# Performance work log

Measured on AMD Instinct MI355X. Metric: run time of the kernel, lower is better.

## Reference

```python
import jax, jax.numpy as jnp
import numpy as np

N_TOKENS = 2048
HIDDEN = 1024
INTER = 2816
N_EXPERTS = 8
N_ADAPTERS = 2
MAX_RANK = 16
TOP_K = 2
N_SEQS = 8


def setup_inputs() -> dict:
    key = jax.random.key(0)
    ks = jax.random.split(key, 12)
    f32 = jnp.float32
    std = 0.02
    hidden_states = jax.random.normal(ks[0], (N_TOKENS, HIDDEN), f32)
    topk_ids = jax.random.randint(ks[1], (N_TOKENS, TOP_K), 0, N_EXPERTS)
    tw = jax.random.uniform(ks[2], (N_TOKENS, TOP_K), dtype=f32)
    topk_weights = tw / tw.sum(axis=-1, keepdims=True)
    gate_a = jax.random.normal(ks[3], (N_ADAPTERS, N_EXPERTS, MAX_RANK, HIDDEN), f32) * std
    gate_b = jax.random.normal(ks[4], (N_ADAPTERS, N_EXPERTS, INTER, MAX_RANK), f32) * std
    up_a = jax.random.normal(ks[5], (N_ADAPTERS, N_EXPERTS, MAX_RANK, HIDDEN), f32) * std
    up_b = jax.random.normal(ks[6], (N_ADAPTERS, N_EXPERTS, INTER, MAX_RANK), f32) * std
    down_a = jax.random.normal(ks[7], (N_ADAPTERS, N_EXPERTS, MAX_RANK, INTER), f32) * std
    down_b = jax.random.normal(ks[8], (N_ADAPTERS, N_EXPERTS, HIDDEN, MAX_RANK), f32) * std
    weight_indices = jax.random.randint(ks[9], (N_SEQS,), 0, N_ADAPTERS)
    seq_lens = jnp.full((N_SEQS,), N_TOKENS // N_SEQS, dtype=jnp.int32)
    lora_ranks = jnp.array([16, 8], dtype=jnp.int32)
    scalings = jnp.array([2.0, 1.0], dtype=f32)
    base_gate_up_weight = jax.random.normal(ks[10], (N_EXPERTS, 2 * INTER, HIDDEN), f32) * std
    base_down_weight = jax.random.normal(ks[11], (N_EXPERTS, HIDDEN, INTER), f32) * std
    return {
        'hidden_states': hidden_states, 'topk_ids': topk_ids, 'topk_weights': topk_weights,
        'gate_a': gate_a, 'gate_b': gate_b, 'up_a': up_a, 'up_b': up_b,
        'down_a': down_a, 'down_b': down_b, 'weight_indices': weight_indices,
        'seq_lens': seq_lens, 'lora_ranks': lora_ranks, 'scalings': scalings,
        'base_gate_up_weight': base_gate_up_weight, 'base_down_weight': base_down_weight,
    }


def _forward(hidden_states, topk_ids, topk_weights, gate_a, gate_b, up_a, up_b,
             down_a, down_b, weight_indices, seq_lens, lora_ranks, scalings,
             base_gate_up_weight, base_down_weight):
    N, H = hidden_states.shape
    A, E, R, _ = gate_a.shape
    I = gate_b.shape[2]
    x = hidden_states.astype(jnp.float32)
    # token -> sequence -> adapter (replaces the per-token python loop)
    token_to_seq = jnp.searchsorted(jnp.cumsum(seq_lens), jnp.arange(N), side='right')
    adapter = weight_indices[token_to_seq]                               # [N]
    scale_t = scalings[adapter].astype(jnp.float32)[:, None]             # [N,1]
    # per-adapter rank truncation A[:rank] == zeroing rows r >= rank of LoRA-A
    rmask = (jnp.arange(R)[None, :] < lora_ranks[:, None]).astype(jnp.float32)  # [A,R]
    ga = gate_a.astype(jnp.float32) * rmask[:, None, :, None]
    ua = up_a.astype(jnp.float32) * rmask[:, None, :, None]
    da = down_a.astype(jnp.float32) * rmask[:, None, :, None]
    gb = gate_b.astype(jnp.float32)
    ub = up_b.astype(jnp.float32)
    db = down_b.astype(jnp.float32)
    # low-rank input projections for all adapters & experts (tiny: N*A*E*R)
    z_gate = jnp.einsum('nh,aerh->naer', x, ga)
    z_up = jnp.einsum('nh,aerh->naer', x, ua)
    sel = adapter[:, None, None]
    Wgu = base_gate_up_weight.astype(jnp.float32)   # [E, 2I, H]
    Wd = base_down_weight.astype(jnp.float32)       # [E, H, I]
    out = jnp.zeros((N, H), jnp.float32)
    for e in range(E):
        # summed routing weight for this expert per token (0 => no contribution)
        w_e = jnp.where(topk_ids == e, topk_weights, 0.0).sum(axis=1).astype(jnp.float32)  # [N]
        base_gate = x @ Wgu[e, :I].T                 # [N,I]
        base_up = x @ Wgu[e, I:].T                   # [N,I]
        lg = jnp.take_along_axis(jnp.einsum('nar,air->nai', z_gate[:, :, e], gb[:, e]), sel, axis=1)[:, 0]
        lu = jnp.take_along_axis(jnp.einsum('nar,air->nai', z_up[:, :, e], ub[:, e]), sel, axis=1)[:, 0]
        gate_out = base_gate + scale_t * lg
        up_out = base_up + scale_t * lu
        act = jax.nn.silu(gate_out) * up_out         # [N,I]
        zd = jnp.einsum('ni,ari->nar', act, da[:, e])
        ld = jnp.take_along_axis(jnp.einsum('nar,ahr->nah', zd, db[:, e]), sel, axis=1)[:, 0]
        base_down = act @ Wd[e].T                    # [N,H]
        out = out + w_e[:, None] * (base_down + scale_t * ld)
    return out.astype(hidden_states.dtype)


def reference(hidden_states, topk_ids, topk_weights, gate_a, gate_b, up_a, up_b,
              down_a, down_b, weight_indices, seq_lens, lora_ranks, scalings,
              base_gate_up_weight, base_down_weight):
    return _forward(hidden_states, topk_ids, topk_weights, gate_a, gate_b, up_a, up_b,
                    down_a, down_b, weight_indices, seq_lens, lora_ranks, scalings,
                    base_gate_up_weight, base_down_weight)
```

## Files before the change

kernel.cpp:

```cpp
#include <hip/hip_runtime.h>
#include <hip/hip_bf16.h>
#include <math.h>

#define N_TOK   2048
#define HIDDEN  1024
#define INTER   2816
#define NEXP    8
#define NADAPT  2
#define MAXRANK 16
#define TOPK    2
#define NSEQ    8
#define NPAIRS  (N_TOK*TOPK)
#define NGU     (2*INTER)

typedef unsigned short u16;
typedef __attribute__((ext_vector_type(8))) short bf16x8;
typedef __attribute__((ext_vector_type(4))) float f32x4;

#define F_CNT   0u
#define F_PERM  4096u
#define F_ZG    139264u
#define F_ZU    401408u
#define F_ZD    663552u
#define F_XBF   1048576u
#define F_ACT   5242880u
#define F_GB    28311552u
#define F_UB    29753344u
#define F_DB    31195136u
#define F_GA_BF 31719424u
#define F_UA_BF 32243712u
#define F_ZDF   32768000u
#define F_DA_BF 33554432u
#define FAST_NEED 171966464u

#define B_CNT   0u
#define B_PERM  4096u
#define B_ZG    262144u
#define B_ZU    524288u
#define B_ZD    786432u
#define B_ACT   1048576u

__device__ __forceinline__ float bf2f(u16 u){
  union { unsigned int i; float f; } v; v.i = ((unsigned int)u)<<16; return v.f;
}
__device__ __forceinline__ u16 f2bf(float f){
  union { float f; unsigned int i; } v; v.f = f;
  unsigned int i = v.i;
  return (u16)((i + 0x7fffu + ((i>>16)&1u)) >> 16);
}
__device__ __forceinline__ uint4 cvt8(const float* src){
  float4 lo = *(const float4*)src;
  float4 hi = *(const float4*)(src+4);
  uint4 r;
  r.x = (unsigned)f2bf(lo.x) | ((unsigned)f2bf(lo.y)<<16);
  r.y = (unsigned)f2bf(lo.z) | ((unsigned)f2bf(lo.w)<<16);
  r.z = (unsigned)f2bf(hi.x) | ((unsigned)f2bf(hi.y)<<16);
  r.w = (unsigned)f2bf(hi.z) | ((unsigned)f2bf(hi.w)<<16);
  return r;
}
__device__ __forceinline__ uint2 cvt4(float4 v){
  uint2 r;
  r.x = (unsigned)f2bf(v.x) | ((unsigned)f2bf(v.y)<<16);
  r.y = (unsigned)f2bf(v.z) | ((unsigned)f2bf(v.w)<<16);
  return r;
}

__device__ __forceinline__ unsigned cvtpk(float a, float b){
  unsigned r;
  asm("v_cvt_pk_bf16_f32 %0, %1, %2" : "=v"(r) : "v"(a), "v"(b));
  return r;
}
__device__ __forceinline__ uint4 pack8(float4 lo, float4 hi){
  uint4 r;
  r.x = cvtpk(lo.x, lo.y);
  r.y = cvtpk(lo.z, lo.w);
  r.z = cvtpk(hi.x, hi.y);
  r.w = cvtpk(hi.z, hi.w);
  return r;
}

__device__ __forceinline__ void cvt_chunk8k(const float* __restrict__ src, u16* __restrict__ dst, int c, int t){
  size_t b4 = (size_t)c*2048 + t;
  float4 v0 = ((const float4*)src)[b4];
  float4 v1 = ((const float4*)src)[b4 + 256];
  float4 v2 = ((const float4*)src)[b4 + 512];
  float4 v3 = ((const float4*)src)[b4 + 768];
  float4 v4 = ((const float4*)src)[b4 + 1024];
  float4 v5 = ((const float4*)src)[b4 + 1280];
  float4 v6 = ((const float4*)src)[b4 + 1536];
  float4 v7 = ((const float4*)src)[b4 + 1792];
  ((uint2*)dst)[b4]        = cvt4(v0);
  ((uint2*)dst)[b4 + 256]  = cvt4(v1);
  ((uint2*)dst)[b4 + 512]  = cvt4(v2);
  ((uint2*)dst)[b4 + 768]  = cvt4(v3);
  ((uint2*)dst)[b4 + 1024] = cvt4(v4);
  ((uint2*)dst)[b4 + 1280] = cvt4(v5);
  ((uint2*)dst)[b4 + 1536] = cvt4(v6);
  ((uint2*)dst)[b4 + 1792] = cvt4(v7);
}
__device__ __forceinline__ void zero_chunk8k(float* dst, int c, int t){
  size_t b4 = (size_t)c*2048 + t;
  #pragma unroll
  for (int i = 0; i < 8; ++i)
    ((float4*)dst)[b4 + i*256] = make_float4(0.f,0.f,0.f,0.f);
}

__device__ __forceinline__ void gl16(const void* g, void* l){
  __builtin_amdgcn_global_load_lds(
      (const __attribute__((address_space(1))) unsigned int*)g,
      (__attribute__((address_space(3))) unsigned int*)l, 16, 0, 0);
}

__device__ __forceinline__ int token_adapter(int n, const int* seq_lens, const int* widx){
  int cum = 0;
  #pragma unroll
  for (int s = 0; s < NSEQ; ++s){ cum += seq_lens[s]; if (n < cum) return widx[s]; }
  return widx[NSEQ-1];
}

__global__ void k_zero(float* outf, int* cnt, float* zdf){
  int t = threadIdx.x;
  if (blockIdx.x < 2048){
    int id = blockIdx.x*256 + t;
    *(float4*)&outf[(size_t)id*4] = make_float4(0.f,0.f,0.f,0.f);
  } else {
    int id = (blockIdx.x - 2048)*256 + t;
    *(float4*)&zdf[(size_t)id*4] = make_float4(0.f,0.f,0.f,0.f);
  }
  if (blockIdx.x == 0 && t < NEXP) cnt[t] = 0;
}

__global__ void k_route(const int* __restrict__ topk_ids, int* cnt, int* perm){
  int p = blockIdx.x*256 + threadIdx.x;
  if (p >= NPAIRS) return;
  int e = topk_ids[p];
  int pos = atomicAdd(&cnt[e], 1);
  perm[e*NPAIRS + pos] = p;
}

__global__ void k_cvt(const float* __restrict__ src, u16* __restrict__ dst, int n4){
  int id = blockIdx.x*256 + threadIdx.x;
  if (id >= n4) return;
  ((uint2*)dst)[id] = cvt4(((const float4*)src)[id]);
}

__global__ void k_prep(
    const float* __restrict__ x,  const float* __restrict__ gb, const float* __restrict__ ub,
    const float* __restrict__ ga, const float* __restrict__ ua, const float* __restrict__ db_,
    const float* __restrict__ da,
    u16* xb, u16* gbb, u16* ubb, u16* gab, u16* uab, u16* dbb, u16* dab,
    float* outf, float* zdf, int* cnt)
{
  int b = blockIdx.x, t = threadIdx.x;
  if (b == 0 && t < NEXP) cnt[t] = 0;
  if      (b < 256) cvt_chunk8k(x,   xb,  b,       t);
  else if (b < 344) cvt_chunk8k(gb,  gbb, b - 256, t);
  else if (b < 432) cvt_chunk8k(ub,  ubb, b - 344, t);
  else if (b < 464) cvt_chunk8k(ga,  gab, b - 432, t);
  else if (b < 496) cvt_chunk8k(ua,  uab, b - 464, t);
  else if (b < 528) cvt_chunk8k(db_, dbb, b - 496, t);
  else if (b < 616) cvt_chunk8k(da,  dab, b - 528, t);
  else if (b < 872) zero_chunk8k(outf, b - 616, t);
  else              zero_chunk8k(zdf,  b - 872, t);
}

__global__ __launch_bounds__(256) void k_zgu_mfma(
    const u16* __restrict__ xb, const u16* __restrict__ gab, const u16* __restrict__ uab,
    const int* __restrict__ cnt, const int* __restrict__ perm,
    const int* __restrict__ widx, const int* __restrict__ seq_lens,
    const int* __restrict__ ranks, const float* __restrict__ scal,
    u16* __restrict__ zg, u16* __restrict__ zu)
{
  int e = blockIdx.y;
  int me = cnt[e];
  int tm = blockIdx.x;
  if (tm*64 >= me) return;
  int t = threadIdx.x;

  __shared__ __align__(16) u16 As[64*32];
  __shared__ __align__(16) u16 Bs[64*32];

  int r0 = t >> 2;
  int kc = ((t&3) - r0) & 3;
  int ko = kc*8;
  int mg = tm*64 + r0;
  int pa = perm[e*NPAIRS + min(mg, me-1)];
  const u16* arow = xb + (size_t)(pa>>1)*HIDDEN + ko;
  int jr = r0 & 31;
  const u16* brow = (r0 < 32 ? gab : uab)
                    + (size_t)(((jr>>4)*NEXP + e)*MAXRANK + (jr&15))*HIDDEN + ko;

  int wv = t>>6, lane = t&63;
  u16* Asw = &As[wv*512];
  u16* Bsw = &Bs[wv*512];
  int wm = wv>>1, wn = wv&1;
  int l15 = lane&15, q = lane>>4;

  f32x4 acc[2][2] = {};
  int aoff[2], boff[2];
  #pragma unroll
  for (int i=0;i<2;++i){ int row = wm*32 + i*16 + l15; aoff[i] = row*32 + ((q+row)&3)*8; }
  #pragma unroll
  for (int j=0;j<2;++j){ int row = wn*32 + j*16 + l15; boff[j] = row*32 + ((q+row)&3)*8; }

  for (int kt = 0; kt < HIDDEN/32; ++kt){
    __syncthreads();
    gl16(arow + kt*32, Asw);
    gl16(brow + kt*32, Bsw);
    __syncthreads();
    bf16x8 af[2], bfr[2];
    #pragma unroll
    for (int i=0;i<2;++i) af[i] = *(const bf16x8*)&As[aoff[i]];
    #pragma unroll
    for (int j=0;j<2;++j) bfr[j] = *(const bf16x8*)&Bs[boff[j]];
    #pragma unroll
    for (int i=0;i<2;++i)
      #pragma unroll
      for (int j=0;j<2;++j)
        acc[i][j] = __builtin_amdgcn_mfma_f32_16x16x32_bf16(af[i], bfr[j], acc[i][j],0,0,0);
  }

  u16* dstz = wn ? zu : zg;
  #pragma unroll
  for (int i=0;i<2;++i){
    #pragma unroll
    for (int r=0;r<4;++r){
      int mgo = tm*64 + wm*32 + i*16 + q*4 + r;
      if (mgo < me){
        int p = perm[e*NPAIRS + mgo];
        int a = token_adapter(p>>1, seq_lens, widx);
        int rank = ranks[a]; float sc = scal[a];
        #pragma unroll
        for (int j=0;j<2;++j){
          int jc = j*16 + l15;
          float v = ((jc>>4)==a && (jc&15)<rank) ? sc*acc[i][j][r] : 0.f;
          dstz[(size_t)p*32 + jc] = f2bf(v);
        }
      }
    }
  }
}

__global__ __launch_bounds__(256) void k_zd_mfma(
    const u16* __restrict__ act, const u16* __restrict__ dab,
    const int* __restrict__ cnt, const int* __restrict__ perm,
    const int* __restrict__ widx, const int* __restrict__ seq_lens,
    const int* __restrict__ ranks, const float* __restrict__ scal,
    float* __restrict__ zdf)
{
  int e = blockIdx.z;
  int me = cnt[e];
  int tm = blockIdx.y;
  if (tm*64 >= me) return;
  int ks = blockIdx.x;
  int t = threadIdx.x;

  __shared__ __align__(16) u16 As[64*32];
  __shared__ __align__(16) u16 Bs[32*32];

  int r0 = t >> 2;
  int kc = ((t&3) - r0) & 3;
  int ko = kc*8;
  int mg = tm*64 + r0;
  int pa = perm[e*NPAIRS + min(mg, me-1)];
  const u16* arow = act + (size_t)pa*INTER + ko;
  int jr = r0 & 31;
  const u16* brow = dab + (size_t)(((jr>>4)*NEXP + e)*MAXRANK + (jr&15))*INTER + ko;

  int wv = t>>6, lane = t&63;
  u16* Asw = &As[wv*512];
  u16* Bsw = &Bs[(wv&1)*512];
  int l15 = lane&15, q = lane>>4;

  f32x4 acc[2] = {};
  int aoff; { int row = wv*16 + l15; aoff = row*32 + ((q+row)&3)*8; }
  int boff[2];
  #pragma unroll
  for (int j=0;j<2;++j){ int row = j*16 + l15; boff[j] = row*32 + ((q+row)&3)*8; }

  int kt0 = ks*22, kt1 = kt0 + 22;
  for (int kt = kt0; kt < kt1; ++kt){
    __syncthreads();
    gl16(arow + kt*32, Asw);
    if (wv < 2) gl16(brow + kt*32, Bsw);
    __syncthreads();
    bf16x8 af = *(const bf16x8*)&As[aoff];
    bf16x8 b0 = *(const bf16x8*)&Bs[boff[0]];
    bf16x8 b1 = *(const bf16x8*)&Bs[boff[1]];
    acc[0] = __builtin_amdgcn_mfma_f32_16x16x32_bf16(af, b0, acc[0],0,0,0);
    acc[1] = __builtin_amdgcn_mfma_f32_16x16x32_bf16(af, b1, acc[1],0,0,0);
  }

  #pragma unroll
  for (int r=0;r<4;++r){
    int mgo = tm*64 + wv*16 + q*4 + r;
    if (mgo < me){
      int p = perm[e*NPAIRS + mgo];
      int a = token_adapter(p>>1, seq_lens, widx);
      int rank = ranks[a]; float sc = scal[a];
      #pragma unroll
      for (int j=0;j<2;++j){
        int jc = j*16 + l15;
        if ((jc>>4)==a && (jc&15)<rank)
          atomicAdd(&zdf[(size_t)p*32 + jc], sc*acc[j][r]);
      }
    }
  }
}

__global__ __launch_bounds__(256) void k_zgu(
    const float* __restrict__ x, const int* __restrict__ topk_ids,
    const float* __restrict__ gate_a, const float* __restrict__ up_a,
    const int* __restrict__ widx, const int* __restrict__ seq_lens,
    const int* __restrict__ ranks, const float* __restrict__ scal,
    u16* __restrict__ zg, u16* __restrict__ zu)
{
  int p = blockIdx.x, n = p >> 1, t = threadIdx.x;
  int e = topk_ids[p];
  __shared__ float xs[HIDDEN];
  for (int i = t; i < HIDDEN; i += 256) xs[i] = x[(size_t)n*HIDDEN + i];
  if (t < 32){ zg[p*32 + t] = 0; zu[p*32 + t] = 0; }
  __syncthreads();
  int a = token_adapter(n, seq_lens, widx);
  int rank = ranks[a];
  float scale = scal[a];
  int wv = t >> 6, lane = t & 63;
  for (int i = 0; i < 8; ++i){
    int o = wv*8 + i;
    int r = o & 15;
    const float* wrow = ((o < 16) ? gate_a : up_a) + (size_t)((a*NEXP + e)*MAXRANK + r)*HIDDEN;
    float s = 0.f;
    for (int h = lane; h < HIDDEN; h += 64) s += xs[h] * wrow[h];
    s += __shfl_down(s,32); s += __shfl_down(s,16); s += __shfl_down(s,8);
    s += __shfl_down(s,4);  s += __shfl_down(s,2);  s += __shfl_down(s,1);
    if (lane == 0 && r < rank)
      (o < 16 ? zg : zu)[p*32 + a*16 + r] = f2bf(scale * s);
  }
}

__global__ __launch_bounds__(256) void k_zd(
    const u16* __restrict__ act, const int* __restrict__ topk_ids,
    const float* __restrict__ down_a,
    const int* __restrict__ widx, const int* __restrict__ seq_lens,
    const int* __restrict__ ranks, const float* __restrict__ scal,
    u16* __restrict__ zd)
{
  int p = blockIdx.x, n = p >> 1, t = threadIdx.x;
  int e = topk_ids[p];
  __shared__ float as_[INTER];
  for (int i = t; i < INTER; i += 256) as_[i] = bf2f(act[(size_t)p*INTER + i]);
  if (t < 32) zd[p*32 + t] = 0;
  __syncthreads();
  int a = token_adapter(n, seq_lens, widx);
  int rank = ranks[a];
  float scale = scal[a];
  int wv = t >> 6, lane = t & 63;
  for (int i = 0; i < 4; ++i){
    int r = wv*4 + i;
    const float* wrow = down_a + (size_t)((a*NEXP + e)*MAXRANK + r)*INTER;
    float s = 0.f;
    for (int h = lane; h < INTER; h += 64) s += as_[h] * wrow[h];
    s += __shfl_down(s,32); s += __shfl_down(s,16); s += __shfl_down(s,8);
    s += __shfl_down(s,4);  s += __shfl_down(s,2);  s += __shfl_down(s,1);
    if (lane == 0 && r < rank) zd[p*32 + a*16 + r] = f2bf(scale * s);
  }
}

__global__ __launch_bounds__(256) void k_gu_f32(
    const u16* __restrict__ xb, const float* __restrict__ wgu_f32,
    const u16* __restrict__ gbb, const u16* __restrict__ ubb,
    const u16* __restrict__ zg, const u16* __restrict__ zu,
    const int* __restrict__ cnt, const int* __restrict__ perm,
    u16* __restrict__ act)
{
  int e = blockIdx.z;
  int me = cnt[e];
  int tm = blockIdx.y;
  if (tm*128 >= me) return;
  int tn = blockIdx.x;
  int t = threadIdx.x;

  __shared__ __align__(16) u16 As[128*32];
  __shared__ __align__(16) u16 Bg[64*32];
  __shared__ __align__(16) u16 Bu[64*32];

  int r0 = t >> 2;
  int kc = ((t&3) - r0) & 3;
  int ko = kc*8;
  int mg0 = tm*128 + r0, mg1 = mg0 + 64;
  int p0 = perm[e*NPAIRS + min(mg0, me-1)];
  int p1 = perm[e*NPAIRS + min(mg1, me-1)];
  const u16* arow0 = xb + (size_t)(p0>>1)*HIDDEN + ko;
  const u16* arow1 = xb + (size_t)(p1>>1)*HIDDEN + ko;
  int jg = tn*64 + r0;
  const float4* pg = (const float4*)(wgu_f32 + ((size_t)e*NGU + jg)*HIDDEN + ko);
  const float4* pu = (const float4*)(wgu_f32 + ((size_t)e*NGU + INTER + jg)*HIDDEN + ko);

  int wvb = (t>>6)*512;
  u16* Asw0 = &As[wvb];
  u16* Asw1 = &As[2048 + wvb];
  u16* Bgw  = &Bg[wvb];

  int wv = t>>6, lane = t&63;
  int wm = wv>>1, wn = wv&1;
  int l15 = lane&15, q = lane>>4;

  f32x4 accg[4][2] = {};
  f32x4 accu[4][2] = {};
  int aoff[4], boff[2];
  #pragma unroll
  for (int i=0;i<4;++i){ int row = wm*64 + i*16 + l15; aoff[i] = row*32 + ((q+row)&3)*8; }
  #pragma unroll
  for (int j=0;j<2;++j){ int row = wn*32 + j*16 + l15; boff[j] = row*32 + ((q+row)&3)*8; }

  float4 rg0 = pg[0], rg1 = pg[1];
  float4 ru0 = pu[0], ru1 = pu[1];

  for (int kt = 0; kt < HIDDEN/32; ++kt){
    uint4 bg = pack8(rg0, rg1);
    uint4 bu = pack8(ru0, ru1);
    __syncthreads();
    gl16(arow0 + kt*32, Asw0);
    gl16(arow1 + kt*32, Asw1);
    *(uint4*)&Bg[wvb + lane*8] = bg;
    *(uint4*)&Bu[wvb + lane*8] = bu;
    __syncthreads();
    if (kt + 1 < HIDDEN/32){
      int o = (kt+1)*8;
      rg0 = pg[o]; rg1 = pg[o+1]; ru0 = pu[o]; ru1 = pu[o+1];
    }
    bf16x8 af[4], bgf[2], buf[2];
    #pragma unroll
    for (int i=0;i<4;++i) af[i] = *(const bf16x8*)&As[aoff[i]];
    #pragma unroll
    for (int j=0;j<2;++j){ bgf[j] = *(const bf16x8*)&Bg[boff[j]]; buf[j] = *(const bf16x8*)&Bu[boff[j]]; }
    #pragma unroll
    for (int i=0;i<4;++i)
      #pragma unroll
      for (int j=0;j<2;++j){
        accg[i][j] = __builtin_amdgcn_mfma_f32_16x16x32_bf16(af[i], bgf[j], accg[i][j],0,0,0);
        accu[i][j] = __builtin_amdgcn_mfma_f32_16x16x32_bf16(af[i], buf[j], accu[i][j],0,0,0);
      }
  }
  {
    int aid = kc>>1, rr = (kc&1)*8;
    const u16* gB = gbb + ((size_t)(aid*NEXP+e)*INTER + jg)*MAXRANK + rr;
    const u16* uB = ubb + ((size_t)(aid*NEXP+e)*INTER + jg)*MAXRANK + rr;
    __syncthreads();
    gl16(zg + (size_t)p0*32 + ko, Asw0);
    gl16(zg + (size_t)p1*32 + ko, Asw1);
    gl16(gB, Bgw);
    __syncthreads();
    {
      bf16x8 af[4], bgf[2];
      #pragma unroll
      for (int i=0;i<4;++i) af[i] = *(const bf16x8*)&As[aoff[i]];
      #pragma unroll
      for (int j=0;j<2;++j) bgf[j] = *(const bf16x8*)&Bg[boff[j]];
      #pragma unroll
      for (int i=0;i<4;++i)
        #pragma unroll
        for (int j=0;j<2;++j)
          accg[i][j] = __builtin_amdgcn_mfma_f32_16x16x32_bf16(af[i], bgf[j], accg[i][j],0,0,0);
    }
    __syncthreads();
    gl16(zu + (size_t)p0*32 + ko, Asw0);
    gl16(zu + (size_t)p1*32 + ko, Asw1);
    gl16(uB, Bgw);
    __syncthreads();
    {
      bf16x8 af[4], buf[2];
      #pragma unroll
      for (int i=0;i<4;++i) af[i] = *(const bf16x8*)&As[aoff[i]];
      #pragma unroll
      for (int j=0;j<2;++j) buf[j] = *(const bf16x8*)&Bg[boff[j]];
      #pragma unroll
      for (int i=0;i<4;++i)
        #pragma unroll
        for (int j=0;j<2;++j)
          accu[i][j] = __builtin_amdgcn_mfma_f32_16x16x32_bf16(af[i], buf[j], accu[i][j],0,0,0);
    }
  }

  int col = l15, quad = q;
  #pragma unroll
  for (int i = 0; i < 4; ++i){
    #pragma unroll
    for (int r = 0; r < 4; ++r){
      int mg = tm*128 + wm*64 + i*16 + quad*4 + r;
      if (mg < me){
        int p = perm[e*NPAIRS + mg];
        size_t base = (size_t)p*INTER;
        #pragma unroll
        for (int j = 0; j < 2; ++j){
          int jc = tn*64 + wn*32 + j*16 + col;
          float g = accg[i][j][r], u = accu[i][j][r];
          float s = g / (1.f + __expf(-g));
          act[base + jc] = f2bf(s*u);
        }
      }
    }
  }
}

__global__ __launch_bounds__(256) void k_down_f32(
    const u16* __restrict__ act, const float* __restrict__ wd_f32,
    const u16* __restrict__ dbb, const u16* __restrict__ zd,
    const float* __restrict__ tw,
    const int* __restrict__ cnt, const int* __restrict__ perm,
    float* __restrict__ outf)
{
  int e = blockIdx.z;
  int me = cnt[e];
  int tm = blockIdx.y;
  if (tm*128 >= me) return;
  int tn = blockIdx.x & 7;
  int ks = blockIdx.x >> 3;
  int t = threadIdx.x;

  __shared__ __align__(16) u16 As[128*32];
  __shared__ __align__(16) u16 Bs[128*32];

  int r0 = t >> 2;
  int kc = ((t&3) - r0) & 3;
  int ko = kc*8;
  int mg0 = tm*128 + r0, mg1 = mg0 + 64;
  int p0 = perm[e*NPAIRS + min(mg0, me-1)];
  int p1 = perm[e*NPAIRS + min(mg1, me-1)];
  const u16* arow0 = act + (size_t)p0*INTER + ko;
  const u16* arow1 = act + (size_t)p1*INTER + ko;
  int j0 = tn*128 + r0, j1 = j0 + 64;
  const float4* pb0 = (const float4*)(wd_f32 + ((size_t)e*HIDDEN + j0)*INTER + ko);
  const float4* pb1 = (const float4*)(wd_f32 + ((size_t)e*HIDDEN + j1)*INTER + ko);

  int wvb = (t>>6)*512;
  u16* Asw0 = &As[wvb];
  u16* Asw1 = &As[2048 + wvb];
  u16* Bsw0 = &Bs[wvb];
  u16* Bsw1 = &Bs[2048 + wvb];

  int wv = t>>6, lane = t&63;
  int wm = wv>>1, wn = wv&1;
  int l15 = lane&15, q = lane>>4;

  f32x4 acc[4][4] = {};
  int aoff[4], boff[4];
  #pragma unroll
  for (int i=0;i<4;++i){ int row = wm*64 + i*16 + l15; aoff[i] = row*32 + ((q+row)&3)*8; }
  #pragma unroll
  for (int j=0;j<4;++j){ int row = wn*64 + j*16 + l15; boff[j] = row*32 + ((q+row)&3)*8; }

  auto mma = [&](){
    bf16x8 af[4], bfr[4];
    #pragma unroll
    for (int i=0;i<4;++i){ af[i] = *(const bf16x8*)&As[aoff[i]]; bfr[i] = *(const bf16x8*)&Bs[boff[i]]; }
    #pragma unroll
    for (int i=0;i<4;++i)
      #pragma unroll
      for (int j=0;j<4;++j)
        acc[i][j] = __builtin_amdgcn_mfma_f32_16x16x32_bf16(af[i], bfr[j], acc[i][j],0,0,0);
  };

  int kt0 = ks*22, kt1 = kt0 + 22;
  float4 r00 = pb0[kt0*8], r01 = pb0[kt0*8+1];
  float4 r10 = pb1[kt0*8], r11 = pb1[kt0*8+1];
  for (int kt = kt0; kt < kt1; ++kt){
    uint4 b0 = pack8(r00, r01);
    uint4 b1 = pack8(r10, r11);
    __syncthreads();
    gl16(arow0 + kt*32, Asw0);
    gl16(arow1 + kt*32, Asw1);
    *(uint4*)&Bs[wvb + lane*8]        = b0;
    *(uint4*)&Bs[2048 + wvb + lane*8] = b1;
    __syncthreads();
    if (kt + 1 < kt1){
      int o = (kt+1)*8;
      r00 = pb0[o]; r01 = pb0[o+1]; r10 = pb1[o]; r11 = pb1[o+1];
    }
    mma();
  }
  if (ks == 3){
    int aid = kc>>1, rr = (kc&1)*8;
    __syncthreads();
    gl16(zd + (size_t)p0*32 + ko, Asw0);
    gl16(zd + (size_t)p1*32 + ko, Asw1);
    gl16(dbb + ((size_t)(aid*NEXP+e)*HIDDEN + j0)*MAXRANK + rr, Bsw0);
    gl16(dbb + ((size_t)(aid*NEXP+e)*HIDDEN + j1)*MAXRANK + rr, Bsw1);
    __syncthreads();
    mma();
  }

  int col = l15, quad = q;
  #pragma unroll
  for (int i = 0; i < 4; ++i){
    #pragma unroll
    for (int r = 0; r < 4; ++r){
      int mg = tm*128 + wm*64 + i*16 + quad*4 + r;
      if (mg < me){
        int p = perm[e*NPAIRS + mg];
        float wp = tw[p];
        size_t base = (size_t)(p >> 1)*HIDDEN;
        #pragma unroll
        for (int j = 0; j < 4; ++j){
          int jc = tn*128 + wn*64 + j*16 + col;
          atomicAdd(&outf[base + jc], wp * acc[i][j][r]);
        }
      }
    }
  }
}

__global__ __launch_bounds__(256) void k_gufused(
    const float* __restrict__ x, const float* __restrict__ wgu,
    const float* __restrict__ gate_b, const float* __restrict__ up_b,
    const u16* __restrict__ zg, const u16* __restrict__ zu,
    const int* __restrict__ cnt, const int* __restrict__ perm,
    u16* __restrict__ act)
{
  int e = blockIdx.z;
  int me = cnt[e];
  int tm = blockIdx.y;
  if (tm*128 >= me) return;
  int tn = blockIdx.x;
  int t = threadIdx.x;

  __shared__ __align__(16) u16 As[128*32];
  __shared__ __align__(16) u16 Bg[64*32];
  __shared__ __align__(16) u16 Bu[64*32];

  int r0 = t >> 2, cc = t & 3;
  int mg0 = tm*128 + r0, mg1 = mg0 + 64;
  int p0 = perm[e*NPAIRS + min(mg0, me-1)];
  int p1 = perm[e*NPAIRS + min(mg1, me-1)];
  const float* arow0 = x + (size_t)(p0 >> 1)*HIDDEN;
  const float* arow1 = x + (size_t)(p1 >> 1)*HIDDEN;
  int jg = tn*64 + r0;
  const float* browg = wgu + ((size_t)e*NGU + jg)*HIDDEN;
  const float* browu = wgu + ((size_t)e*NGU + INTER + jg)*HIDDEN;

  int wv = t >> 6, lane = t & 63;
  int wm = wv >> 1, wn = wv & 1;

  f32x4 accg[4][2] = {};
  f32x4 accu[4][2] = {};
  int aoff[4], boff[2];
  #pragma unroll
  for (int i = 0; i < 4; ++i) aoff[i] = (wm*64 + i*16 + (lane&15))*32 + (lane>>4)*8;
  #pragma unroll
  for (int j = 0; j < 2; ++j) boff[j] = (wn*32 + j*16 + (lane&15))*32 + (lane>>4)*8;

  for (int kt = 0; kt < HIDDEN/32; ++kt){
    uint4 a0 = cvt8(arow0 + kt*32 + cc*8);
    uint4 a1 = cvt8(arow1 + kt*32 + cc*8);
    uint4 bg = cvt8(browg + kt*32 + cc*8);
    uint4 bu = cvt8(browu + kt*32 + cc*8);
    __syncthreads();
    *(uint4*)&As[r0*32 + cc*8]      = a0;
    *(uint4*)&As[(r0+64)*32 + cc*8] = a1;
    *(uint4*)&Bg[r0*32 + cc*8]      = bg;
    *(uint4*)&Bu[r0*32 + cc*8]      = bu;
    __syncthreads();
    bf16x8 af[4], bgf[2], buf[2];
    #pragma unroll
    for (int i = 0; i < 4; ++i) af[i] = *(const bf16x8*)&As[aoff[i]];
    #pragma unroll
    for (int j = 0; j < 2; ++j){ bgf[j] = *(const bf16x8*)&Bg[boff[j]]; buf[j] = *(const bf16x8*)&Bu[boff[j]]; }
    #pragma unroll
    for (int i = 0; i < 4; ++i)
      #pragma unroll
      for (int j = 0; j < 2; ++j){
        accg[i][j] = __builtin_amdgcn_mfma_f32_16x16x32_bf16(af[i], bgf[j], accg[i][j], 0, 0, 0);
        accu[i][j] = __builtin_amdgcn_mfma_f32_16x16x32_bf16(af[i], buf[j], accu[i][j], 0, 0, 0);
      }
  }
  {
    uint4 a0 = *(const uint4*)(zg + (size_t)p0*32 + cc*8);
    uint4 a1 = *(const uint4*)(zg + (size_t)p1*32 + cc*8);
    int aid = cc >> 1, rr = (cc & 1)*8;
    uint4 bg = cvt8(gate_b + ((size_t)(aid*NEXP + e)*INTER + jg)*MAXRANK + rr);
    __syncthreads();
    *(uint4*)&As[r0*32 + cc*8]      = a0;
    *(uint4*)&As[(r0+64)*32 + cc*8] = a1;
    *(uint4*)&Bg[r0*32 + cc*8]      = bg;
    __syncthreads();
    bf16x8 af[4], bgf[2];
    #pragma unroll
    for (int i = 0; i < 4; ++i) af[i] = *(const bf16x8*)&As[aoff[i]];
    #pragma unroll
    for (int j = 0; j < 2; ++j) bgf[j] = *(const bf16x8*)&Bg[boff[j]];
    #pragma unroll
    for (int i = 0; i < 4; ++i)
      #pragma unroll
      for (int j = 0; j < 2; ++j)
        accg[i][j] = __builtin_amdgcn_mfma_f32_16x16x32_bf16(af[i], bgf[j], accg[i][j], 0, 0, 0);
  }
  {
    uint4 a0 = *(const uint4*)(zu + (size_t)p0*32 + cc*8);
    uint4 a1 = *(const uint4*)(zu + (size_t)p1*32 + cc*8);
    int aid = cc >> 1, rr = (cc & 1)*8;
    uint4 bu = cvt8(up_b + ((size_t)(aid*NEXP + e)*INTER + jg)*MAXRANK + rr);
    __syncthreads();
    *(uint4*)&As[r0*32 + cc*8]      = a0;
    *(uint4*)&As[(r0+64)*32 + cc*8] = a1;
    *(uint4*)&Bg[r0*32 + cc*8]      = bu;
    __syncthreads();
    bf16x8 af[4], buf[2];
    #pragma unroll
    for (int i = 0; i < 4; ++i) af[i] = *(const bf16x8*)&As[aoff[i]];
    #pragma unroll
    for (int j = 0; j < 2; ++j) buf[j] = *(const bf16x8*)&Bg[boff[j]];
    #pragma unroll
    for (int i = 0; i < 4; ++i)
      #pragma unroll
      for (int j = 0; j < 2; ++j)
        accu[i][j] = __builtin_amdgcn_mfma_f32_16x16x32_bf16(af[i], buf[j], accu[i][j], 0, 0, 0);
  }
  int col = lane & 15, quad = lane >> 4;
  #pragma unroll
  for (int i = 0; i < 4; ++i){
    #pragma unroll
    for (int r = 0; r < 4; ++r){
      int mg = tm*128 + wm*64 + i*16 + quad*4 + r;
      if (mg < me){
        int p = perm[e*NPAIRS + mg];
        size_t base = (size_t)p*INTER;
        #pragma unroll
        for (int j = 0; j < 2; ++j){
          int jc = tn*64 + wn*32 + j*16 + col;
          float g = accg[i][j][r], u = accu[i][j][r];
          float s = g / (1.f + __expf(-g));
          act[base + jc] = f2bf(s*u);
        }
      }
    }
  }
}

__global__ __launch_bounds__(256) void k_gemm_down(
    const u16* __restrict__ act, const float* __restrict__ wd,
    const float* __restrict__ down_b, const u16* __restrict__ zd,
    const float* __restrict__ tw,
    const int* __restrict__ cnt, const int* __restrict__ perm,
    float* __restrict__ outf)
{
  int e = blockIdx.z;
  int me = cnt[e];
  int tm = blockIdx.y;
  if (tm*128 >= me) return;
  int tn = blockIdx.x;
  int t = threadIdx.x;

  __shared__ __align__(16) u16 As[128*32];
  __shared__ __align__(16) u16 Bs[128*32];

  int r0 = t >> 2, cc = t & 3;
  int mg0 = tm*128 + r0, mg1 = mg0 + 64;
  int p0 = perm[e*NPAIRS + min(mg0, me-1)];
  int p1 = perm[e*NPAIRS + min(mg1, me-1)];
  const u16* arow0 = act + (size_t)p0*INTER;
  const u16* arow1 = act + (size_t)p1*INTER;
  int j0 = tn*128 + r0, j1 = j0 + 64;
  const float* brow0 = wd + ((size_t)e*HIDDEN + j0)*INTER;
  const float* brow1 = wd + ((size_t)e*HIDDEN + j1)*INTER;

  int wv = t >> 6, lane = t & 63;
  int wm = wv >> 1, wn = wv & 1;

  f32x4 acc[4][4] = {};
  int aoff[4], boff[4];
  #pragma unroll
  for (int i = 0; i < 4; ++i){
    aoff[i] = (wm*64 + i*16 + (lane&15))*32 + (lane>>4)*8;
    boff[i] = (wn*64 + i*16 + (lane&15))*32 + (lane>>4)*8;
  }

  auto compute = [&](){
    bf16x8 af[4], bfr[4];
    #pragma unroll
    for (int i = 0; i < 4; ++i){
      af[i]  = *(const bf16x8*)&As[aoff[i]];
      bfr[i] = *(const bf16x8*)&Bs[boff[i]];
    }
    #pragma unroll
    for (int i = 0; i < 4; ++i)
      #pragma unroll
      for (int j = 0; j < 4; ++j)
        acc[i][j] = __builtin_amdgcn_mfma_f32_16x16x32_bf16(af[i], bfr[j], acc[i][j], 0, 0, 0);
  };

  for (int kt = 0; kt < INTER/32; ++kt){
    uint4 a0 = *(const uint4*)(arow0 + kt*32 + cc*8);
    uint4 a1 = *(const uint4*)(arow1 + kt*32 + cc*8);
    uint4 b0 = cvt8(brow0 + kt*32 + cc*8);
    uint4 b1 = cvt8(brow1 + kt*32 + cc*8);
    __syncthreads();
    *(uint4*)&As[r0*32 + cc*8]      = a0;
    *(uint4*)&As[(r0+64)*32 + cc*8] = a1;
    *(uint4*)&Bs[r0*32 + cc*8]      = b0;
    *(uint4*)&Bs[(r0+64)*32 + cc*8] = b1;
    __syncthreads();
    compute();
  }
  {
    uint4 a0 = *(const uint4*)(zd + (size_t)p0*32 + cc*8);
    uint4 a1 = *(const uint4*)(zd + (size_t)p1*32 + cc*8);
    int aid = cc >> 1, rr = (cc & 1)*8;
    uint4 b0 = cvt8(down_b + ((size_t)(aid*NEXP + e)*HIDDEN + j0)*MAXRANK + rr);
    uint4 b1 = cvt8(down_b + ((size_t)(aid*NEXP + e)*HIDDEN + j1)*MAXRANK + rr);
    __syncthreads();
    *(uint4*)&As[r0*32 + cc*8]      = a0;
    *(uint4*)&As[(r0+64)*32 + cc*8] = a1;
    *(uint4*)&Bs[r0*32 + cc*8]      = b0;
    *(uint4*)&Bs[(r0+64)*32 + cc*8] = b1;
    __syncthreads();
    compute();
  }
  int col = lane & 15, quad = lane >> 4;
  #pragma unroll
  for (int i = 0; i < 4; ++i){
    #pragma unroll
    for (int r = 0; r < 4; ++r){
      int mg = tm*128 + wm*64 + i*16 + quad*4 + r;
      if (mg < me){
        int p = perm[e*NPAIRS + mg];
        float wp = tw[p];
        size_t base = (size_t)(p >> 1)*HIDDEN;
        #pragma unroll
        for (int j = 0; j < 4; ++j){
          int jc = tn*128 + wn*64 + j*16 + col;
          atomicAdd(&outf[base + jc], wp * acc[i][j][r]);
        }
      }
    }
  }
}

extern "C" void kernel_launch(void* const* d_in, const int* in_sizes, int n_in,
                              void* d_out, int out_size, void* d_ws, size_t ws_size,
                              hipStream_t stream){
  const float* x        = (const float*)d_in[0];
  const int*   topk_ids = (const int*)d_in[1];
  const float* tw       = (const float*)d_in[2];
  const float* gate_a   = (const float*)d_in[3];
  const float* gate_b   = (const float*)d_in[4];
  const float* up_a     = (const float*)d_in[5];
  const float* up_b     = (const float*)d_in[6];
  const float* down_a   = (const float*)d_in[7];
  const float* down_b   = (const float*)d_in[8];
  const int*   widx     = (const int*)d_in[9];
  const int*   seq_lens = (const int*)d_in[10];
  const int*   ranks    = (const int*)d_in[11];
  const float* scal     = (const float*)d_in[12];
  const float* wgu      = (const float*)d_in[13];
  const float* wd       = (const float*)d_in[14];
  float* outf = (float*)d_out;
  char* ws = (char*)d_ws;

  if (ws_size >= (size_t)FAST_NEED){
    int* cnt  = (int*)(ws + F_CNT);
    int* perm = (int*)(ws + F_PERM);
    u16* zg   = (u16*)(ws + F_ZG);
    u16* zu   = (u16*)(ws + F_ZU);
    u16* zd   = (u16*)(ws + F_ZD);
    u16* xb   = (u16*)(ws + F_XBF);
    u16* act  = (u16*)(ws + F_ACT);
    u16* gbb  = (u16*)(ws + F_GB);
    u16* ubb  = (u16*)(ws + F_UB);
    u16* dbb  = (u16*)(ws + F_DB);
    u16* gab  = (u16*)(ws + F_GA_BF);
    u16* uab  = (u16*)(ws + F_UA_BF);
    float* zdf= (float*)(ws + F_ZDF);
    u16* dab  = (u16*)(ws + F_DA_BF);

    hipLaunchKernelGGL(k_prep, dim3(888), dim3(256), 0, stream,
                       x, gate_b, up_b, gate_a, up_a, down_b, down_a,
                       xb, gbb, ubb, gab, uab, dbb, dab, outf, zdf, cnt);
    hipLaunchKernelGGL(k_route, dim3(16), dim3(256), 0, stream, topk_ids, cnt, perm);
    hipLaunchKernelGGL(k_zgu_mfma, dim3(64, NEXP), dim3(256), 0, stream,
                       xb, gab, uab, cnt, perm, widx, seq_lens, ranks, scal, zg, zu);
    hipLaunchKernelGGL(k_gu_f32, dim3(INTER/64, 32, NEXP), dim3(256), 0, stream,
                       xb, wgu, gbb, ubb, zg, zu, cnt, perm, act);
    hipLaunchKernelGGL(k_zd_mfma, dim3(4, 64, NEXP), dim3(256), 0, stream,
                       act, dab, cnt, perm, widx, seq_lens, ranks, scal, zdf);
    hipLaunchKernelGGL(k_cvt, dim3((NPAIRS*32/4+255)/256), dim3(256), 0, stream,
                       zdf, zd, NPAIRS*32/4);
    hipLaunchKernelGGL(k_down_f32, dim3(32, 32, NEXP), dim3(256), 0, stream,
                       act, wd, dbb, zd, tw, cnt, perm, outf);
  } else {
    int* cnt  = (int*)(ws + B_CNT);
    int* perm = (int*)(ws + B_PERM);
    u16* zg   = (u16*)(ws + B_ZG);
    u16* zu   = (u16*)(ws + B_ZU);
    u16* zd   = (u16*)(ws + B_ZD);
    u16* act  = (u16*)(ws + B_ACT);

    hipLaunchKernelGGL(k_zero,  dim3(2048), dim3(256), 0, stream, outf, cnt, outf);
    hipLaunchKernelGGL(k_route, dim3(16), dim3(256), 0, stream, topk_ids, cnt, perm);
    hipLaunchKernelGGL(k_zgu,   dim3(NPAIRS), dim3(256), 0, stream,
                       x, topk_ids, gate_a, up_a, widx, seq_lens, ranks, scal, zg, zu);
    hipLaunchKernelGGL(k_gufused, dim3(INTER/64, 32, NEXP), dim3(256), 0, stream,
                       x, wgu, gate_b, up_b, zg, zu, cnt, perm, act);
    hipLaunchKernelGGL(k_zd,    dim3(NPAIRS), dim3(256), 0, stream,
                       act, topk_ids, down_a, widx, seq_lens, ranks, scal, zd);
    hipLaunchKernelGGL(k_gemm_down, dim3(HIDDEN/128, 32, NEXP), dim3(256), 0, stream,
                       act, wd, down_b, zd, tw, cnt, perm, outf);
  }
}
```

Baseline: 604.4 us.

## Remap GEMM grids to XCD-aware 1D order and drop register prefetch

The gate/up and down GEMM kernels now run on a flat 1D grid whose block index is decoded so that all M-tiles sharing the same weight column tile (and expert) land on the same XCD. The goal is for each XCD's L2 to serve the fp32 weight tile across all token tiles instead of refetching it from HBM. The register double-buffer prefetch of the next weight slice is also removed, so loads are issued inside each iteration just before the barrier. That frees registers but exposes global load latency within every K step.

```diff
diff --git a/kernel.cpp b/kernel.cpp
--- a/kernel.cpp
+++ b/kernel.cpp
@@ -373,11 +373,14 @@
     const int* __restrict__ cnt, const int* __restrict__ perm,
     u16* __restrict__ act)
 {
-  int e = blockIdx.z;
+  int id = blockIdx.x;
+  int xcd = id & 7, s = id >> 3;
+  int tm = s & 31;
+  int P = (s >> 5)*8 + xcd;
+  int tn = P % 44;
+  int e  = P / 44;
   int me = cnt[e];
-  int tm = blockIdx.y;
   if (tm*128 >= me) return;
-  int tn = blockIdx.x;
   int t = threadIdx.x;
 
   __shared__ __align__(16) u16 As[128*32];
@@ -413,22 +416,18 @@
   #pragma unroll
   for (int j=0;j<2;++j){ int row = wn*32 + j*16 + l15; boff[j] = row*32 + ((q+row)&3)*8; }
 
-  float4 rg0 = pg[0], rg1 = pg[1];
-  float4 ru0 = pu[0], ru1 = pu[1];
-
   for (int kt = 0; kt < HIDDEN/32; ++kt){
-    uint4 bg = pack8(rg0, rg1);
-    uint4 bu = pack8(ru0, ru1);
+    int o = kt*8;
+    float4 g0 = pg[o], g1 = pg[o+1];
+    float4 u0 = pu[o], u1 = pu[o+1];
+    uint4 bg = pack8(g0, g1);
+    uint4 bu = pack8(u0, u1);
     __syncthreads();
     gl16(arow0 + kt*32, Asw0);
     gl16(arow1 + kt*32, Asw1);
     *(uint4*)&Bg[wvb + lane*8] = bg;
     *(uint4*)&Bu[wvb + lane*8] = bu;
     __syncthreads();
-    if (kt + 1 < HIDDEN/32){
-      int o = (kt+1)*8;
-      rg0 = pg[o]; rg1 = pg[o+1]; ru0 = pu[o]; ru1 = pu[o+1];
-    }
     bf16x8 af[4], bgf[2], buf[2];
     #pragma unroll
     for (int i=0;i<4;++i) af[i] = *(const bf16x8*)&As[aoff[i]];
@@ -510,12 +509,15 @@
     const int* __restrict__ cnt, const int* __restrict__ perm,
     float* __restrict__ outf)
 {
-  int e = blockIdx.z;
+  int id = blockIdx.x;
+  int xcd = id & 7, s = id >> 3;
+  int tm = s & 31;
+  int P = (s >> 5)*8 + xcd;
+  int tn = P & 7;
+  int ks = (P >> 3) & 3;
+  int e  = P >> 5;
   int me = cnt[e];
-  int tm = blockIdx.y;
   if (tm*128 >= me) return;
-  int tn = blockIdx.x & 7;
-  int ks = blockIdx.x >> 3;
   int t = threadIdx.x;
 
   __shared__ __align__(16) u16 As[128*32];
@@ -562,21 +564,18 @@
   };
 
   int kt0 = ks*22, kt1 = kt0 + 22;
-  float4 r00 = pb0[kt0*8], r01 = pb0[kt0*8+1];
-  float4 r10 = pb1[kt0*8], r11 = pb1[kt0*8+1];
   for (int kt = kt0; kt < kt1; ++kt){
-    uint4 b0 = pack8(r00, r01);
-    uint4 b1 = pack8(r10, r11);
+    int o = kt*8;
+    float4 a0 = pb0[o], a1 = pb0[o+1];
+    float4 c0 = pb1[o], c1 = pb1[o+1];
+    uint4 b0 = pack8(a0, a1);
+    uint4 b1 = pack8(c0, c1);
     __syncthreads();
     gl16(arow0 + kt*32, Asw0);
     gl16(arow1 + kt*32, Asw1);
     *(uint4*)&Bs[wvb + lane*8]        = b0;
     *(uint4*)&Bs[2048 + wvb + lane*8] = b1;
     __syncthreads();
-    if (kt + 1 < kt1){
-      int o = (kt+1)*8;
-      r00 = pb0[o]; r01 = pb0[o+1]; r10 = pb1[o]; r11 = pb1[o+1];
-    }
     mma();
   }
   if (ks == 3){
@@ -878,13 +877,13 @@
     hipLaunchKernelGGL(k_route, dim3(16), dim3(256), 0, stream, topk_ids, cnt, perm);
     hipLaunchKernelGGL(k_zgu_mfma, dim3(64, NEXP), dim3(256), 0, stream,
                        xb, gab, uab, cnt, perm, widx, seq_lens, ranks, scal, zg, zu);
-    hipLaunchKernelGGL(k_gu_f32, dim3(INTER/64, 32, NEXP), dim3(256), 0, stream,
+    hipLaunchKernelGGL(k_gu_f32, dim3(44*32*NEXP), dim3(256), 0, stream,
                        xb, wgu, gbb, ubb, zg, zu, cnt, perm, act);
     hipLaunchKernelGGL(k_zd_mfma, dim3(4, 64, NEXP), dim3(256), 0, stream,
                        act, dab, cnt, perm, widx, seq_lens, ranks, scal, zdf);
     hipLaunchKernelGGL(k_cvt, dim3((NPAIRS*32/4+255)/256), dim3(256), 0, stream,
                        zdf, zd, NPAIRS*32/4);
-    hipLaunchKernelGGL(k_down_f32, dim3(32, 32, NEXP), dim3(256), 0, stream,
+    hipLaunchKernelGGL(k_down_f32, dim3(8*4*32*NEXP), dim3(256), 0, stream,
                        act, wd, dbb, zd, tw, cnt, perm, outf);
   } else {
     int* cnt  = (int*)(ws + B_CNT);
```

Result: no change. 615.4 us (+1.8%).
